# Kernel optimization log

Measured on AMD Instinct MI355X. Metric: run time of the kernel, lower is better.

Reference implementation:

```python
import jax, jax.numpy as jnp
import numpy as np
from jax import lax

RADIUS = 32
STRIDE = RADIUS // 2
EPS = 1e-4
DN = ('NCHW', 'OIHW', 'NCHW')


def _upsample_bilinear_ac(x, H, W):
    # align_corners=True bilinear resize of NCHW x to (H, W), separable gather.
    b, c, h, w = x.shape
    ys = jnp.linspace(0.0, h - 1, H)
    xs = jnp.linspace(0.0, w - 1, W)
    y0 = jnp.floor(ys).astype(jnp.int32)
    y1 = jnp.minimum(y0 + 1, h - 1)
    wy = (ys - y0.astype(x.dtype)).astype(x.dtype)
    x0 = jnp.floor(xs).astype(jnp.int32)
    x1 = jnp.minimum(x0 + 1, w - 1)
    wx = (xs - x0.astype(x.dtype)).astype(x.dtype)
    rows = x[:, :, y0, :] * (1 - wy)[None, None, :, None] + x[:, :, y1, :] * wy[None, None, :, None]
    out = rows[:, :, :, x0] * (1 - wx) + rows[:, :, :, x1] * wx
    return out


def reference(guide, src, w1, w3):
    B, _, H, W = guide.shape
    f32 = guide.dtype

    def box3(x):  # depthwise strided box-sum (all-ones weights)
        return lax.conv_general_dilated(x, w3, (STRIDE, STRIDE), 'VALID',
                                        dimension_numbers=DN, feature_group_count=3)

    def box1(x):  # learned 1-channel strided conv
        return lax.conv_general_dilated(x, w1, (STRIDE, STRIDE), 'VALID',
                                        dimension_numbers=DN)

    gr, gg, gb = guide[:, 0:1], guide[:, 1:2], guide[:, 2:3]
    N = box1(jnp.ones_like(gr))                     # [B,1,h,w]
    mean_I = box3(guide) / N                        # [B,3,h,w]
    mIr, mIg, mIb = mean_I[:, 0:1], mean_I[:, 1:2], mean_I[:, 2:3]
    mean_p = box3(src) / N                          # [B,3,h,w]

    cov_r = box3(gr * src) / N - mIr * mean_p       # [B,3,h,w]
    cov_g = box3(gg * src) / N - mIg * mean_p
    cov_b = box3(gb * src) / N - mIb * mean_p

    v_rr = box1(gr * gr) / N - mIr * mIr + EPS
    v_rg = box1(gr * gg) / N - mIr * mIg
    v_rb = box1(gr * gb) / N - mIr * mIb
    v_gg = box1(gg * gg) / N - mIg * mIg + EPS
    v_gb = box1(gg * gb) / N - mIg * mIb
    v_bb = box1(gb * gb) / N - mIb * mIb + EPS

    det = (v_rr * v_gg * v_bb + v_rg * v_gb * v_rb + v_rb * v_rg * v_gb
           - v_rb * v_gg * v_rb - v_rg * v_rg * v_bb - v_rr * v_gb * v_gb)

    i_rr = (v_gg * v_bb - v_gb * v_gb) / det
    i_rg = -(v_rg * v_bb - v_rb * v_gb) / det
    i_rb = (v_rg * v_gb - v_rb * v_gg) / det
    i_gg = (v_rr * v_bb - v_rb * v_rb) / det
    i_gb = -(v_rr * v_gb - v_rb * v_rg) / det
    i_bb = (v_rr * v_gg - v_rg * v_rg) / det

    # inv_sigma: [B,3,3,h,w] (each i_* is [B,1,h,w] -> concat on channel)
    row_r = jnp.concatenate([i_rr, i_rg, i_rb], axis=1)
    row_g = jnp.concatenate([i_rg, i_gg, i_gb], axis=1)
    row_b = jnp.concatenate([i_rb, i_gb, i_bb], axis=1)
    inv_sigma = jnp.stack([row_r, row_g, row_b], axis=1)

    cov_Ip = jnp.stack([cov_r, cov_g, cov_b], axis=1)   # [B,3(i),3(c),h,w]
    A = jnp.einsum('bichw,bijhw->bjchw', cov_Ip, inv_sigma)  # [B,3(j),3(c),h,w]

    b_map = mean_p - A[:, 0] * mIr - A[:, 1] * mIg - A[:, 2] * mIb  # [B,3,h,w]

    h, w = A.shape[-2], A.shape[-1]
    mean_A = _upsample_bilinear_ac(A.reshape(B, 9, h, w), H, W).reshape(B, 3, 3, H, W)
    mean_b = _upsample_bilinear_ac(b_map, H, W)

    # q_c = sum_j A_{j,c} * guide_j + b_c
    return jnp.einsum('bjchw,bjhw->bchw', mean_A, guide) + mean_b


def setup_inputs() -> dict:
    key = jax.random.key(0)
    k1, k2, k3 = jax.random.split(key, 3)
    guide = jax.random.uniform(k1, (8, 3, 1024, 1024), dtype=jnp.float32)
    src = jax.random.uniform(k2, (8, 3, 1024, 1024), dtype=jnp.float32)
    w1 = jax.random.uniform(k3, (1, 1, RADIUS, RADIUS), dtype=jnp.float32)
    w3 = jnp.ones((3, 1, RADIUS, RADIUS), dtype=jnp.float32)
    return {"guide": guide, "src": src, "w1": w1, "w3": w3}
```

## Files before the change

### kernel.cpp

```cpp
#include <hip/hip_runtime.h>

#define HLO 63
#define HFULL 1024
#define GF_EPS 1e-4f
#define LOPLANE (HLO*HLO)
#define NQ 64
#define NSTAT 40

template<int CTRL>
__device__ __forceinline__ float dppadd(float v) {
    int r = __builtin_amdgcn_update_dpp(0, __float_as_int(v), CTRL, 0xF, 0xF, false);
    return v + __int_as_float(r);
}

__global__ __launch_bounds__(256) void gf_vstats(
    const float* __restrict__ guide, const float* __restrict__ src,
    const float* __restrict__ w1, float* __restrict__ hs)
{
    __shared__ float w1s[1024];
    __shared__ float red[4][NSTAT][16];

    int bid = blockIdx.x;
    int chunk = bid & 3;
    int qy    = (bid >> 2) & 63;
    int b     = bid >> 8;
    int tid   = threadIdx.x;
    int lane  = tid & 63;
    int qtr   = tid >> 6;

    reinterpret_cast<float4*>(w1s)[tid] = reinterpret_cast<const float4*>(w1)[tid];
    __syncthreads();

    const size_t plane = (size_t)HFULL * HFULL;
    const size_t rowoff = (size_t)(qy * 16 + qtr * 4) * HFULL + chunk * 256 + lane * 4;
    const float* g0 = guide + (size_t)b * 3 * plane + rowoff;
    const float* s0 = src   + (size_t)b * 3 * plane + rowoff;

    int xq = lane & 3;

    float acc[NSTAT];
#pragma unroll
    for (int i = 0; i < NSTAT; i++) acc[i] = 0.f;

#pragma unroll
    for (int r = 0; r < 4; ++r) {
        size_t off = (size_t)r * HFULL;
        float4 vgr = *reinterpret_cast<const float4*>(g0 + off);
        float4 vgg = *reinterpret_cast<const float4*>(g0 + plane + off);
        float4 vgb = *reinterpret_cast<const float4*>(g0 + 2 * plane + off);
        float4 vpr = *reinterpret_cast<const float4*>(s0 + off);
        float4 vpg = *reinterpret_cast<const float4*>(s0 + plane + off);
        float4 vpb = *reinterpret_cast<const float4*>(s0 + 2 * plane + off);
        const float* wr = &w1s[(qtr * 4 + r) * 32 + 4 * xq];
        float4 w00 = *reinterpret_cast<const float4*>(wr);
        float4 w01 = *reinterpret_cast<const float4*>(wr + 16);
        float4 w10 = *reinterpret_cast<const float4*>(wr + 512);
        float4 w11 = *reinterpret_cast<const float4*>(wr + 528);

        const float* grf = reinterpret_cast<const float*>(&vgr);
        const float* ggf = reinterpret_cast<const float*>(&vgg);
        const float* gbf = reinterpret_cast<const float*>(&vgb);
        const float* prf = reinterpret_cast<const float*>(&vpr);
        const float* pgf = reinterpret_cast<const float*>(&vpg);
        const float* pbf = reinterpret_cast<const float*>(&vpb);
        const float* w00f = reinterpret_cast<const float*>(&w00);
        const float* w01f = reinterpret_cast<const float*>(&w01);
        const float* w10f = reinterpret_cast<const float*>(&w10);
        const float* w11f = reinterpret_cast<const float*>(&w11);

#pragma unroll
        for (int j = 0; j < 4; ++j) {
            float Gr = grf[j], Gg = ggf[j], Gb = gbf[j];
            float Pr = prf[j], Pg = pgf[j], Pb = pbf[j];
            float W00 = w00f[j], W01 = w01f[j], W10 = w10f[j], W11 = w11f[j];

            acc[0] += Gr;  acc[1] += Gg;  acc[2] += Gb;
            acc[3] += Pr;  acc[4] += Pg;  acc[5] += Pb;
            acc[6]  += Gr * Pr;  acc[7]  += Gr * Pg;  acc[8]  += Gr * Pb;
            acc[9]  += Gg * Pr;  acc[10] += Gg * Pg;  acc[11] += Gg * Pb;
            acc[12] += Gb * Pr;  acc[13] += Gb * Pg;  acc[14] += Gb * Pb;

            float RR = Gr * Gr, RG = Gr * Gg, RB = Gr * Gb;
            float GG = Gg * Gg, GB = Gg * Gb, BB = Gb * Gb;
            acc[15] += W00 * RR;  acc[16] += W01 * RR;  acc[17] += W10 * RR;  acc[18] += W11 * RR;
            acc[19] += W00 * RG;  acc[20] += W01 * RG;  acc[21] += W10 * RG;  acc[22] += W11 * RG;
            acc[23] += W00 * RB;  acc[24] += W01 * RB;  acc[25] += W10 * RB;  acc[26] += W11 * RB;
            acc[27] += W00 * GG;  acc[28] += W01 * GG;  acc[29] += W10 * GG;  acc[30] += W11 * GG;
            acc[31] += W00 * GB;  acc[32] += W01 * GB;  acc[33] += W10 * GB;  acc[34] += W11 * GB;
            acc[35] += W00 * BB;  acc[36] += W01 * BB;  acc[37] += W10 * BB;  acc[38] += W11 * BB;
            acc[39] += (W00 + W01) + (W10 + W11);
        }
    }

#pragma unroll
    for (int i = 0; i < NSTAT; i++) {
        acc[i] = dppadd<0xB1>(acc[i]);
        acc[i] = dppadd<0x4E>(acc[i]);
    }

    if ((lane & 3) == 0) {
        int k16 = lane >> 2;
#pragma unroll
        for (int i = 0; i < NSTAT; i++)
            red[qtr][i][k16] = acc[i];
    }
    __syncthreads();

    for (int i = tid; i < NSTAT * 16; i += 256) {
        int stat = i >> 4, k16 = i & 15;
        float sum = red[0][stat][k16] + red[1][stat][k16]
                  + red[2][stat][k16] + red[3][stat][k16];
        hs[((size_t)(b * NQ + qy) * NSTAT + stat) * 64 + chunk * 16 + k16] = sum;
    }
}

__global__ __launch_bounds__(256) void gf_solve(
    const float* __restrict__ hs, float* __restrict__ ab)
{
    int idx = blockIdx.x * 256 + threadIdx.x;
    if (idx >= 8 * LOPLANE) return;
    int lx = idx % HLO;
    int t  = idx / HLO;
    int ly = t % HLO;
    int b  = t / HLO;

    const float* h0 = hs + ((size_t)b * NQ + ly) * NSTAT * 64;
    const float* h1 = h0 + (size_t)NSTAT * 64;

    float s[15];
#pragma unroll
    for (int i = 0; i < 15; i++) {
        int o = i * 64 + lx;
        s[i] = (h0[o] + h0[o + 1]) + (h1[o] + h1[o + 1]);
    }

    float v[6];
#pragma unroll
    for (int p = 0; p < 6; p++) {
        int base = 15 + p * 4;
        v[p] = h0[(base + 0) * 64 + lx]
             + h0[(base + 1) * 64 + lx + 1]
             + h1[(base + 2) * 64 + lx]
             + h1[(base + 3) * 64 + lx + 1];
    }
    float N = h0[39 * 64 + lx];

    float inv_n = 1.f / N;
    float mI[3] = { s[0] * inv_n, s[1] * inv_n, s[2] * inv_n };
    float mp[3] = { s[3] * inv_n, s[4] * inv_n, s[5] * inv_n };

    float cov[3][3];
#pragma unroll
    for (int i = 0; i < 3; i++)
#pragma unroll
        for (int c = 0; c < 3; c++)
            cov[i][c] = s[6 + i * 3 + c] * inv_n - mI[i] * mp[c];

    float v_rr = v[0] * inv_n - mI[0] * mI[0] + GF_EPS;
    float v_rg = v[1] * inv_n - mI[0] * mI[1];
    float v_rb = v[2] * inv_n - mI[0] * mI[2];
    float v_gg = v[3] * inv_n - mI[1] * mI[1] + GF_EPS;
    float v_gb = v[4] * inv_n - mI[1] * mI[2];
    float v_bb = v[5] * inv_n - mI[2] * mI[2] + GF_EPS;

    float det = v_rr * v_gg * v_bb + v_rg * v_gb * v_rb + v_rb * v_rg * v_gb
              - v_rb * v_gg * v_rb - v_rg * v_rg * v_bb - v_rr * v_gb * v_gb;
    float invdet = 1.f / det;

    float i_rr =  (v_gg * v_bb - v_gb * v_gb) * invdet;
    float i_rg = -(v_rg * v_bb - v_rb * v_gb) * invdet;
    float i_rb =  (v_rg * v_gb - v_rb * v_gg) * invdet;
    float i_gg =  (v_rr * v_bb - v_rb * v_rb) * invdet;
    float i_gb = -(v_rr * v_gb - v_rb * v_rg) * invdet;
    float i_bb =  (v_rr * v_gg - v_rg * v_rg) * invdet;

    float inv[3][3] = { { i_rr, i_rg, i_rb },
                        { i_rg, i_gg, i_gb },
                        { i_rb, i_gb, i_bb } };

    float A[3][3];
#pragma unroll
    for (int j = 0; j < 3; j++)
#pragma unroll
        for (int c = 0; c < 3; c++)
            A[j][c] = inv[j][0] * cov[0][c] + inv[j][1] * cov[1][c] + inv[j][2] * cov[2][c];

    float bb_[3];
#pragma unroll
    for (int c = 0; c < 3; c++)
        bb_[c] = mp[c] - A[0][c] * mI[0] - A[1][c] * mI[1] - A[2][c] * mI[2];

    float* outp = ab + (size_t)b * 12 * LOPLANE + ly * HLO + lx;
#pragma unroll
    for (int j = 0; j < 3; j++)
#pragma unroll
        for (int c = 0; c < 3; c++)
            outp[(j * 3 + c) * LOPLANE] = A[j][c];
#pragma unroll
    for (int c = 0; c < 3; c++)
        outp[(9 + c) * LOPLANE] = bb_[c];
}

__global__ __launch_bounds__(256) void gf_apply(
    const float* __restrict__ guide, const float* __restrict__ ab,
    float* __restrict__ out)
{
    __shared__ float rl[12][64];

    int bid = blockIdx.x;
    int y = bid & 1023;
    int b = bid >> 10;
    int tid = threadIdx.x;

    const float scale = 62.0f / 1023.0f;
    float ty = (float)y * scale;
    int y0 = (int)ty;  if (y0 > 61) y0 = 61;
    float wy = ty - (float)y0;

    const float* abb = ab + (size_t)b * 12 * LOPLANE;
    for (int i = tid; i < 12 * 63; i += 256) {
        int p = i / 63, c = i - p * 63;
        const float* pp = abb + (size_t)p * LOPLANE + y0 * HLO + c;
        rl[p][c] = pp[0] * (1.f - wy) + pp[HLO] * wy;
    }
    __syncthreads();

    int x = 4 * tid;
    float t0 = (float)x * scale;
    int c0 = (int)t0;  if (c0 > 61) c0 = 61;

    bool  sel[4];
    float wx[4];
#pragma unroll
    for (int j = 0; j < 4; ++j) {
        float t = (float)(x + j) * scale;
        int x0 = (int)t;  if (x0 > 61) x0 = 61;
        sel[j] = (x0 > c0);
        wx[j]  = t - (float)x0;
    }

    float Av[12][4];
#pragma unroll
    for (int p = 0; p < 12; ++p) {
        float r0 = rl[p][c0], r1 = rl[p][c0 + 1], r2 = rl[p][c0 + 2];
#pragma unroll
        for (int j = 0; j < 4; ++j) {
            float a  = sel[j] ? r1 : r0;
            float bb = sel[j] ? r2 : r1;
            Av[p][j] = a + (bb - a) * wx[j];
        }
    }

    const size_t plane = (size_t)HFULL * HFULL;
    size_t goff = (size_t)b * 3 * plane + ((size_t)y << 10) + x;
    float4 vgr = *reinterpret_cast<const float4*>(guide + goff);
    float4 vgg = *reinterpret_cast<const float4*>(guide + goff + plane);
    float4 vgb = *reinterpret_cast<const float4*>(guide + goff + 2 * plane);
    const float* grf = reinterpret_cast<const float*>(&vgr);
    const float* ggf = reinterpret_cast<const float*>(&vgg);
    const float* gbf = reinterpret_cast<const float*>(&vgb);

#pragma unroll
    for (int c = 0; c < 3; ++c) {
        float4 o;
        float* of = reinterpret_cast<float*>(&o);
#pragma unroll
        for (int j = 0; j < 4; ++j)
            of[j] = Av[0 + c][j] * grf[j] + Av[3 + c][j] * ggf[j]
                  + Av[6 + c][j] * gbf[j] + Av[9 + c][j];
        *reinterpret_cast<float4*>(out + goff + (size_t)c * plane) = o;
    }
}

extern "C" void kernel_launch(void* const* d_in, const int* in_sizes, int n_in,
                              void* d_out, int out_size, void* d_ws, size_t ws_size,
                              hipStream_t stream) {
    const float* guide = (const float*)d_in[0];
    const float* src   = (const float*)d_in[1];
    const float* w1    = (const float*)d_in[2];
    float* out = (float*)d_out;

    float* ab = (float*)d_ws;
    float* hs = (float*)((char*)d_ws + (2 << 20));

    gf_vstats<<<8 * NQ * 4, 256, 0, stream>>>(guide, src, w1, hs);

    int nthr = 8 * LOPLANE;
    gf_solve<<<(nthr + 255) / 256, 256, 0, stream>>>(hs, ab);

    gf_apply<<<8 * 1024, 256, 0, stream>>>(guide, ab, out);
}
```

Measured before the change: 75.80 us.

## Stage stats inputs via global_load_lds DMA, split rows, and tile solve through LDS

The stats kernel now launches twice as many blocks, each covering 8 rows instead of 16. Each block pulls its six input planes into shared memory with async global_load_lds DMA, then computes from LDS, and writes two half-row partial sums per quad row. The solve kernel now gives one block per low-res row: it cooperatively loads both quad rows' partials into shared memory and combines the halves. The aim is more memory parallelism and occupancy in the bandwidth-bound stats pass. The cost is more LDS per block (about 56KB, which limits occupancy) and extra partial-sum traffic, and most solve threads sit idle.

```diff
diff --git a/kernel.cpp b/kernel.cpp
--- a/kernel.cpp
+++ b/kernel.cpp
@@ -13,29 +13,49 @@
     return v + __int_as_float(r);
 }
 
+__device__ __forceinline__ void dma16(const float* g, float* l) {
+    __builtin_amdgcn_global_load_lds(
+        (const __attribute__((address_space(1))) unsigned int*)g,
+        (__attribute__((address_space(3))) unsigned int*)l,
+        16, 0, 0);
+}
+
 __global__ __launch_bounds__(256) void gf_vstats(
     const float* __restrict__ guide, const float* __restrict__ src,
     const float* __restrict__ w1, float* __restrict__ hs)
 {
+    __shared__ float data[6][8][256];
     __shared__ float w1s[1024];
     __shared__ float red[4][NSTAT][16];
 
     int bid = blockIdx.x;
     int chunk = bid & 3;
-    int qy    = (bid >> 2) & 63;
-    int b     = bid >> 8;
+    int h     = (bid >> 2) & 1;
+    int qy    = (bid >> 3) & 63;
+    int b     = bid >> 9;
     int tid   = threadIdx.x;
     int lane  = tid & 63;
-    int qtr   = tid >> 6;
+    int wv    = tid >> 6;
 
     reinterpret_cast<float4*>(w1s)[tid] = reinterpret_cast<const float4*>(w1)[tid];
+
+    const size_t plane = (size_t)HFULL * HFULL;
+    const float* g0 = guide + (size_t)b * 3 * plane
+                    + (size_t)(qy * 16 + h * 8) * HFULL + chunk * 256;
+    const float* s0 = src   + (size_t)b * 3 * plane
+                    + (size_t)(qy * 16 + h * 8) * HFULL + chunk * 256;
+
+#pragma unroll
+    for (int ff = 0; ff < 12; ++ff) {
+        int f = wv * 12 + ff;
+        int p = f >> 3, r = f & 7;
+        const float* gp = (p < 3 ? g0 + (size_t)p * plane
+                                 : s0 + (size_t)(p - 3) * plane)
+                        + (size_t)r * HFULL + lane * 4;
+        dma16(gp, &data[p][r][0]);
+    }
     __syncthreads();
 
-    const size_t plane = (size_t)HFULL * HFULL;
-    const size_t rowoff = (size_t)(qy * 16 + qtr * 4) * HFULL + chunk * 256 + lane * 4;
-    const float* g0 = guide + (size_t)b * 3 * plane + rowoff;
-    const float* s0 = src   + (size_t)b * 3 * plane + rowoff;
-
     int xq = lane & 3;
 
     float acc[NSTAT];
@@ -43,19 +63,21 @@
     for (int i = 0; i < NSTAT; i++) acc[i] = 0.f;
 
 #pragma unroll
-    for (int r = 0; r < 4; ++r) {
-        size_t off = (size_t)r * HFULL;
-        float4 vgr = *reinterpret_cast<const float4*>(g0 + off);
-        float4 vgg = *reinterpret_cast<const float4*>(g0 + plane + off);
-        float4 vgb = *reinterpret_cast<const float4*>(g0 + 2 * plane + off);
-        float4 vpr = *reinterpret_cast<const float4*>(s0 + off);
-        float4 vpg = *reinterpret_cast<const float4*>(s0 + plane + off);
-        float4 vpb = *reinterpret_cast<const float4*>(s0 + 2 * plane + off);
-        const float* wr = &w1s[(qtr * 4 + r) * 32 + 4 * xq];
-        float4 w00 = *reinterpret_cast<const float4*>(wr);
-        float4 w01 = *reinterpret_cast<const float4*>(wr + 16);
-        float4 w10 = *reinterpret_cast<const float4*>(wr + 512);
-        float4 w11 = *reinterpret_cast<const float4*>(wr + 528);
+    for (int rr = 0; rr < 2; ++rr) {
+        int row = wv * 2 + rr;
+        int yin = h * 8 + row;
+        float4 vgr = *reinterpret_cast<const float4*>(&data[0][row][lane * 4]);
+        float4 vgg = *reinterpret_cast<const float4*>(&data[1][row][lane * 4]);
+        float4 vgb = *reinterpret_cast<const float4*>(&data[2][row][lane * 4]);
+        float4 vpr = *reinterpret_cast<const float4*>(&data[3][row][lane * 4]);
+        float4 vpg = *reinterpret_cast<const float4*>(&data[4][row][lane * 4]);
+        float4 vpb = *reinterpret_cast<const float4*>(&data[5][row][lane * 4]);
+
+        const float* wr_ = &w1s[yin * 32 + 4 * xq];
+        float4 w00 = *reinterpret_cast<const float4*>(wr_);
+        float4 w01 = *reinterpret_cast<const float4*>(wr_ + 16);
+        float4 w10 = *reinterpret_cast<const float4*>(wr_ + 512);
+        float4 w11 = *reinterpret_cast<const float4*>(wr_ + 528);
 
         const float* grf = reinterpret_cast<const float*>(&vgr);
         const float* ggf = reinterpret_cast<const float*>(&vgg);
@@ -102,7 +124,7 @@
         int k16 = lane >> 2;
 #pragma unroll
         for (int i = 0; i < NSTAT; i++)
-            red[qtr][i][k16] = acc[i];
+            red[wv][i][k16] = acc[i];
     }
     __syncthreads();
 
@@ -110,40 +132,55 @@
         int stat = i >> 4, k16 = i & 15;
         float sum = red[0][stat][k16] + red[1][stat][k16]
                   + red[2][stat][k16] + red[3][stat][k16];
-        hs[((size_t)(b * NQ + qy) * NSTAT + stat) * 64 + chunk * 16 + k16] = sum;
+        hs[(((size_t)(b * NQ + qy) * 2 + h) * NSTAT + stat) * 64 + chunk * 16 + k16] = sum;
     }
 }
 
 __global__ __launch_bounds__(256) void gf_solve(
     const float* __restrict__ hs, float* __restrict__ ab)
 {
-    int idx = blockIdx.x * 256 + threadIdx.x;
-    if (idx >= 8 * LOPLANE) return;
-    int lx = idx % HLO;
-    int t  = idx / HLO;
-    int ly = t % HLO;
-    int b  = t / HLO;
-
-    const float* h0 = hs + ((size_t)b * NQ + ly) * NSTAT * 64;
-    const float* h1 = h0 + (size_t)NSTAT * 64;
+    __shared__ float hl[4][NSTAT][64];
+
+    int bid = blockIdx.x;
+    int ly = bid % HLO;
+    int b  = bid / HLO;
+    int tid = threadIdx.x;
+
+    const float4* srcA = reinterpret_cast<const float4*>(
+        hs + ((size_t)(b * NQ + ly) * 2) * NSTAT * 64);
+    const float4* srcB = reinterpret_cast<const float4*>(
+        hs + ((size_t)(b * NQ + ly + 1) * 2) * NSTAT * 64);
+    float4* dstA = reinterpret_cast<float4*>(&hl[0][0][0]);
+    float4* dstB = reinterpret_cast<float4*>(&hl[2][0][0]);
+
+#pragma unroll
+    for (int i = 0; i < 5; ++i) {
+        int o = i * 256 + tid;
+        dstA[o] = srcA[o];
+        dstB[o] = srcB[o];
+    }
+    __syncthreads();
+
+    if (tid >= HLO) return;
+    int lx = tid;
 
     float s[15];
 #pragma unroll
     for (int i = 0; i < 15; i++) {
-        int o = i * 64 + lx;
-        s[i] = (h0[o] + h0[o + 1]) + (h1[o] + h1[o + 1]);
+        s[i] = ((hl[0][i][lx] + hl[1][i][lx]) + (hl[0][i][lx + 1] + hl[1][i][lx + 1]))
+             + ((hl[2][i][lx] + hl[3][i][lx]) + (hl[2][i][lx + 1] + hl[3][i][lx + 1]));
     }
 
     float v[6];
 #pragma unroll
     for (int p = 0; p < 6; p++) {
-        int base = 15 + p * 4;
-        v[p] = h0[(base + 0) * 64 + lx]
-             + h0[(base + 1) * 64 + lx + 1]
-             + h1[(base + 2) * 64 + lx]
-             + h1[(base + 3) * 64 + lx + 1];
-    }
-    float N = h0[39 * 64 + lx];
+        int bs = 15 + p * 4;
+        v[p] = (hl[0][bs + 0][lx]     + hl[1][bs + 0][lx])
+             + (hl[0][bs + 1][lx + 1] + hl[1][bs + 1][lx + 1])
+             + (hl[2][bs + 2][lx]     + hl[3][bs + 2][lx])
+             + (hl[2][bs + 3][lx + 1] + hl[3][bs + 3][lx + 1]);
+    }
+    float N = hl[0][39][lx] + hl[1][39][lx];
 
     float inv_n = 1.f / N;
     float mI[3] = { s[0] * inv_n, s[1] * inv_n, s[2] * inv_n };
@@ -283,10 +320,9 @@
     float* ab = (float*)d_ws;
     float* hs = (float*)((char*)d_ws + (2 << 20));
 
-    gf_vstats<<<8 * NQ * 4, 256, 0, stream>>>(guide, src, w1, hs);
-
-    int nthr = 8 * LOPLANE;
-    gf_solve<<<(nthr + 255) / 256, 256, 0, stream>>>(hs, ab);
+    gf_vstats<<<8 * NQ * 2 * 4, 256, 0, stream>>>(guide, src, w1, hs);
+
+    gf_solve<<<8 * HLO, 256, 0, stream>>>(hs, ab);
 
     gf_apply<<<8 * 1024, 256, 0, stream>>>(guide, ab, out);
 }
```

New measurement: 86.61 us. +14.3%, slower.
